# Performance work log

Measured on AMD Instinct MI355X. Metric: run time of the kernel, lower is better.

## Reference

```python
import jax, jax.numpy as jnp
import numpy as np

L = 4      # num_layers
H = 8      # nhead
D = 128    # d_model
FF = 256   # dim_feedforward
V = 16     # vocab_size
S = 1024   # window_size (== seq_len, mask is built at this size)
B = 8      # batch
LW = 128   # local attention window (+- LW)
EPS = 1e-5 # torch LayerNorm default


def setup_inputs() -> dict:
    key = jax.random.key(0)
    ks = jax.random.split(key, 8)
    n = lambda k, shape, s=0.02: jax.random.normal(k, shape, dtype=jnp.float32) * s
    return {
        "token_batch": jax.random.randint(ks[0], (B, S), 0, V, dtype=jnp.int32),
        "emb": n(ks[1], (V, D), 1.0),
        "Wqkv": n(ks[2], (L, 3 * D, D)), "bqkv": jnp.zeros((L, 3 * D)),
        "Wo": n(ks[3], (L, D, D)), "bo": jnp.zeros((L, D)),
        "ln1_g": jnp.ones((L, D)), "ln1_b": jnp.zeros((L, D)),
        "ln2_g": jnp.ones((L, D)), "ln2_b": jnp.zeros((L, D)),
        "W1": n(ks[4], (L, FF, D)), "b1": jnp.zeros((L, FF)),
        "W2": n(ks[5], (L, D, FF)), "b2": jnp.zeros((L, D)),
        "lnf_g": jnp.ones((D,)), "lnf_b": jnp.zeros((D,)),
        "Wout": n(ks[6], (1, D)), "bout": jnp.zeros((1,)),
    }


def _ln(x, g, b):
    m = jnp.mean(x, axis=-1, keepdims=True)
    v = jnp.var(x, axis=-1, keepdims=True)
    return (x - m) / jnp.sqrt(v + EPS) * g + b


def _pos_encoding(seq_len, d_model):
    pos = jnp.arange(seq_len, dtype=jnp.float32)[:, None]
    div = jnp.exp(jnp.arange(0, d_model, 2, dtype=jnp.float32) * (-jnp.log(10000.0) / d_model))
    pe = jnp.zeros((seq_len, d_model), dtype=jnp.float32)
    pe = pe.at[:, 0::2].set(jnp.sin(pos * div))
    pe = pe.at[:, 1::2].set(jnp.cos(pos * div))
    return pe


def reference(token_batch, emb, Wqkv, bqkv, Wo, bo, ln1_g, ln1_b, ln2_g, ln2_b,
              W1, b1, W2, b2, lnf_g, lnf_b, Wout, bout):
    Bn, Sn = token_batch.shape
    Dm = emb.shape[1]
    hd = Dm // H
    # embedding + sinusoidal positions (dropout is identity in eval mode)
    x = emb[token_batch] + _pos_encoding(Sn, Dm)[None]  # [B,S,D]
    # local band mask: 0 inside +-LW, -inf outside (as in _create_local_attention_mask)
    i = jnp.arange(Sn)
    mask = jnp.where(jnp.abs(i[:, None] - i[None, :]) <= LW, 0.0, -jnp.inf)  # [S,S]
    for l in range(Wqkv.shape[0]):
        # post-norm TransformerEncoderLayer, relu activation (torch defaults)
        qkv = x @ Wqkv[l].T + bqkv[l]
        q, k, v = jnp.split(qkv, 3, axis=-1)
        q = q.reshape(Bn, Sn, H, hd)
        k = k.reshape(Bn, Sn, H, hd)
        v = v.reshape(Bn, Sn, H, hd)
        scores = jnp.einsum('bqhd,bkhd->bhqk', q, k) / jnp.sqrt(jnp.float32(hd)) + mask
        attn = jax.nn.softmax(scores, axis=-1)
        ctx = jnp.einsum('bhqk,bkhd->bqhd', attn, v).reshape(Bn, Sn, Dm)
        x = _ln(x + ctx @ Wo[l].T + bo[l], ln1_g[l], ln1_b[l])
        ff = jax.nn.relu(x @ W1[l].T + b1[l]) @ W2[l].T + b2[l]
        x = _ln(x + ff, ln2_g[l], ln2_b[l])
    x = _ln(x, lnf_g, lnf_b)
    out = jax.nn.softplus(x @ Wout.T + bout)  # [B,S,1]
    return out[..., 0]
```

## Files before the change

### kernel.cpp

```cpp
#include <hip/hip_runtime.h>
#include <hip/hip_bf16.h>
#include <math.h>

#define NL   4
#define NH   8
#define DM   128
#define FFD  256
#define SEQ  1024
#define BATCH 8
#define NT   (BATCH*SEQ)
#define EPSV 1e-5f

typedef _Float16 h16;
typedef h16   h16x8 __attribute__((ext_vector_type(8)));
typedef float f32x4 __attribute__((ext_vector_type(4)));

#define WQKV_OFF 0
#define WO_OFF   196608
#define W1_OFF   262144
#define W2_OFF   393216
#define WTOT     524288

__global__ __launch_bounds__(256) void cvtw_kernel(
    const float* __restrict__ wqkv, const float* __restrict__ wo,
    const float* __restrict__ w1, const float* __restrict__ w2,
    h16* __restrict__ dst)
{
    int i = (blockIdx.x * 256 + threadIdx.x) * 4;
    const float* src; int off;
    if (i < WO_OFF)      { src = wqkv; off = 0; }
    else if (i < W1_OFF) { src = wo;   off = WO_OFF; }
    else if (i < W2_OFF) { src = w1;   off = W1_OFF; }
    else                 { src = w2;   off = W2_OFF; }
    float4 v = *(const float4*)&src[i - off];
    h16 o[4] = {(h16)v.x, (h16)v.y, (h16)v.z, (h16)v.w};
    *(uint2*)&dst[i] = *(uint2*)o;
}

__global__ __launch_bounds__(256) void embed_kernel(
    const int* __restrict__ tok, const float* __restrict__ emb,
    float* __restrict__ x, h16* __restrict__ xh)
{
    int idx = blockIdx.x * 256 + threadIdx.x;
    int t = idx >> 7;
    int d = idx & 127;
    int s = t & (SEQ - 1);
    int token = tok[t];
    float freq = expf((float)(d & ~1) * (-9.210340371976184f / 128.0f));
    float ang = (float)s * freq;
    float pe = (d & 1) ? cosf(ang) : sinf(ang);
    float v = emb[token * DM + d] + pe;
    x[idx] = v;
    xh[idx] = (h16)v;
}

__global__ __launch_bounds__(256) void gemm16_kernel(
    const h16* __restrict__ A, const h16* __restrict__ W,
    const float* __restrict__ bias, h16* __restrict__ out16, int N)
{
    __shared__ h16 Al[64 * 136];
    __shared__ h16 Wl[64 * 136];

    int tid = threadIdx.x;
    long row0 = (long)blockIdx.x * 64;
    long col0 = (long)blockIdx.y * 64;

    for (int idx = tid; idx < 64 * 16; idx += 256) {
        int r = idx >> 4, c = idx & 15;
        *(uint4*)&Al[r * 136 + c * 8] = *(const uint4*)&A[(row0 + r) * 128 + c * 8];
        *(uint4*)&Wl[r * 136 + c * 8] = *(const uint4*)&W[(col0 + r) * 128 + c * 8];
    }
    __syncthreads();

    int lane = tid & 63, wv = tid >> 6;
    int lr = lane & 15, lg = lane >> 4;
    int wr = (wv >> 1) * 32, wc = (wv & 1) * 32;

    f32x4 acc[2][2] = {{{0.f,0.f,0.f,0.f},{0.f,0.f,0.f,0.f}},
                       {{0.f,0.f,0.f,0.f},{0.f,0.f,0.f,0.f}}};

    #pragma unroll
    for (int k0 = 0; k0 < 128; k0 += 32) {
        h16x8 a0 = *(const h16x8*)&Al[(wr +      lr) * 136 + k0 + lg * 8];
        h16x8 a1 = *(const h16x8*)&Al[(wr + 16 + lr) * 136 + k0 + lg * 8];
        h16x8 b0 = *(const h16x8*)&Wl[(wc +      lr) * 136 + k0 + lg * 8];
        h16x8 b1 = *(const h16x8*)&Wl[(wc + 16 + lr) * 136 + k0 + lg * 8];
        acc[0][0] = __builtin_amdgcn_mfma_f32_16x16x32_f16(a0, b0, acc[0][0], 0, 0, 0);
        acc[0][1] = __builtin_amdgcn_mfma_f32_16x16x32_f16(a0, b1, acc[0][1], 0, 0, 0);
        acc[1][0] = __builtin_amdgcn_mfma_f32_16x16x32_f16(a1, b0, acc[1][0], 0, 0, 0);
        acc[1][1] = __builtin_amdgcn_mfma_f32_16x16x32_f16(a1, b1, acc[1][1], 0, 0, 0);
    }

    #pragma unroll
    for (int m = 0; m < 2; ++m)
    #pragma unroll
    for (int n = 0; n < 2; ++n) {
        long col = col0 + wc + 16 * n + lr;
        float bv = bias[col];
        #pragma unroll
        for (int r = 0; r < 4; ++r) {
            long row = row0 + wr + 16 * m + lg * 4 + r;
            out16[row * N + col] = (h16)(acc[m][n][r] + bv);
        }
    }
}

__device__ __forceinline__ void ln_epilogue(
    f32x4 acc[4], long row0, int wrow, int wcol, int lg, int lr, int w,
    const float* __restrict__ bias, const float* __restrict__ g,
    const float* __restrict__ bb, const float* __restrict__ xres,
    float* __restrict__ xo, h16* __restrict__ xho, float (*red)[2][2])
{
    float val[4][4];
    float bv[4];
    #pragma unroll
    for (int n = 0; n < 4; ++n) bv[n] = bias[wcol + 16 * n + lr];
    #pragma unroll
    for (int r = 0; r < 4; ++r) {
        long row = row0 + wrow + lg * 4 + r;
        #pragma unroll
        for (int n = 0; n < 4; ++n)
            val[r][n] = acc[n][r] + bv[n] + xres[row * 128 + wcol + 16 * n + lr];
    }
    float s[4], sq[4];
    #pragma unroll
    for (int r = 0; r < 4; ++r) {
        s[r]  = val[r][0] + val[r][1] + val[r][2] + val[r][3];
        sq[r] = val[r][0]*val[r][0] + val[r][1]*val[r][1]
              + val[r][2]*val[r][2] + val[r][3]*val[r][3];
        #pragma unroll
        for (int m = 1; m < 16; m <<= 1) {
            s[r]  += __shfl_xor(s[r], m);
            sq[r] += __shfl_xor(sq[r], m);
        }
    }
    int cg = w & 1;
    if (lr == 0) {
        #pragma unroll
        for (int r = 0; r < 4; ++r) {
            red[wrow + lg * 4 + r][cg][0] = s[r];
            red[wrow + lg * 4 + r][cg][1] = sq[r];
        }
    }
    __syncthreads();
    #pragma unroll
    for (int r = 0; r < 4; ++r) {
        int rowt = wrow + lg * 4 + r;
        float S  = red[rowt][0][0] + red[rowt][1][0];
        float SQ = red[rowt][0][1] + red[rowt][1][1];
        float mean = S * (1.0f / 128.0f);
        float var  = SQ * (1.0f / 128.0f) - mean * mean;
        float rstd = rsqrtf(var + EPSV);
        long row = row0 + rowt;
        #pragma unroll
        for (int n = 0; n < 4; ++n) {
            int col = wcol + 16 * n + lr;
            float o = (val[r][n] - mean) * rstd * g[col] + bb[col];
            xo[row * 128 + col]  = o;
            xho[row * 128 + col] = (h16)o;
        }
    }
}

__global__ __launch_bounds__(256) void wo_ln_kernel(
    const h16* __restrict__ ctx, const h16* __restrict__ Wo,
    const float* __restrict__ bo,
    const float* __restrict__ g, const float* __restrict__ bb,
    float* __restrict__ x, h16* __restrict__ xh)
{
    __shared__ h16 Xl[32 * 136];
    __shared__ h16 Wl[128 * 136];
    __shared__ float red[32][2][2];

    int tid = threadIdx.x;
    long row0 = (long)blockIdx.x * 32;

    for (int idx = tid; idx < 32 * 16; idx += 256) {
        int r = idx >> 4, c = idx & 15;
        *(uint4*)&Xl[r * 136 + c * 8] = *(const uint4*)&ctx[(row0 + r) * 128 + c * 8];
    }
    for (int idx = tid; idx < 128 * 16; idx += 256) {
        int r = idx >> 4, c = idx & 15;
        *(uint4*)&Wl[r * 136 + c * 8] = *(const uint4*)&Wo[r * 128 + c * 8];
    }
    __syncthreads();

    int lane = tid & 63, w = tid >> 6;
    int lr = lane & 15, lg = lane >> 4;
    int wrow = (w >> 1) * 16, wcol = (w & 1) * 64;

    f32x4 acc[4] = {{0.f,0.f,0.f,0.f},{0.f,0.f,0.f,0.f},
                    {0.f,0.f,0.f,0.f},{0.f,0.f,0.f,0.f}};
    #pragma unroll
    for (int k0 = 0; k0 < 128; k0 += 32) {
        h16x8 af = *(const h16x8*)&Xl[(wrow + lr) * 136 + k0 + lg * 8];
        #pragma unroll
        for (int n = 0; n < 4; ++n) {
            h16x8 bf = *(const h16x8*)&Wl[(wcol + 16 * n + lr) * 136 + k0 + lg * 8];
            acc[n] = __builtin_amdgcn_mfma_f32_16x16x32_f16(af, bf, acc[n], 0, 0, 0);
        }
    }

    ln_epilogue(acc, row0, wrow, wcol, lg, lr, w, bo, g, bb, x, x, xh, red);
}

__global__ __launch_bounds__(256) void ff_ln_kernel(
    const h16* __restrict__ xh_in, const float* __restrict__ xres,
    const h16* __restrict__ W1, const float* __restrict__ b1,
    const h16* __restrict__ W2, const float* __restrict__ b2,
    const float* __restrict__ g, const float* __restrict__ bb,
    float* __restrict__ x_out, h16* __restrict__ xh_out)
{
    __shared__ h16 Xl[32 * 136];
    __shared__ h16 Wl[128 * 136];
    __shared__ h16 Al[32 * 136];
    __shared__ float red[32][2][2];

    int tid = threadIdx.x;
    long row0 = (long)blockIdx.x * 32;

    for (int idx = tid; idx < 32 * 16; idx += 256) {
        int r = idx >> 4, c = idx & 15;
        *(uint4*)&Xl[r * 136 + c * 8] = *(const uint4*)&xh_in[(row0 + r) * 128 + c * 8];
    }

    int lane = tid & 63, w = tid >> 6;
    int lr = lane & 15, lg = lane >> 4;
    int wrow = (w >> 1) * 16, wcol = (w & 1) * 64;

    f32x4 acc2[4] = {{0.f,0.f,0.f,0.f},{0.f,0.f,0.f,0.f},
                     {0.f,0.f,0.f,0.f},{0.f,0.f,0.f,0.f}};

    #pragma unroll 1
    for (int half = 0; half < 2; ++half) {
        __syncthreads();
        for (int idx = tid; idx < 128 * 16; idx += 256) {
            int r = idx >> 4, c = idx & 15;
            *(uint4*)&Wl[r * 136 + c * 8] =
                *(const uint4*)&W1[(128 * half + r) * 128 + c * 8];
        }
        __syncthreads();

        f32x4 acc1[4] = {{0.f,0.f,0.f,0.f},{0.f,0.f,0.f,0.f},
                         {0.f,0.f,0.f,0.f},{0.f,0.f,0.f,0.f}};
        #pragma unroll
        for (int k0 = 0; k0 < 128; k0 += 32) {
            h16x8 af = *(const h16x8*)&Xl[(wrow + lr) * 136 + k0 + lg * 8];
            #pragma unroll
            for (int n = 0; n < 4; ++n) {
                h16x8 bf = *(const h16x8*)&Wl[(wcol + 16 * n + lr) * 136 + k0 + lg * 8];
                acc1[n] = __builtin_amdgcn_mfma_f32_16x16x32_f16(af, bf, acc1[n], 0, 0, 0);
            }
        }
        __syncthreads();

        #pragma unroll
        for (int r = 0; r < 4; ++r)
            #pragma unroll
            for (int n = 0; n < 4; ++n) {
                int col = wcol + 16 * n + lr;
                float v = acc1[n][r] + b1[128 * half + col];
                Al[(wrow + lg * 4 + r) * 136 + col] = (h16)fmaxf(v, 0.f);
            }
        for (int idx = tid; idx < 128 * 16; idx += 256) {
            int r = idx >> 4, c = idx & 15;
            *(uint4*)&Wl[r * 136 + c * 8] =
                *(const uint4*)&W2[r * 256 + 128 * half + c * 8];
        }
        __syncthreads();

        #pragma unroll
        for (int k0 = 0; k0 < 128; k0 += 32) {
            h16x8 af = *(const h16x8*)&Al[(wrow + lr) * 136 + k0 + lg * 8];
            #pragma unroll
            for (int n = 0; n < 4; ++n) {
                h16x8 bf = *(const h16x8*)&Wl[(wcol + 16 * n + lr) * 136 + k0 + lg * 8];
                acc2[n] = __builtin_amdgcn_mfma_f32_16x16x32_f16(af, bf, acc2[n], 0, 0, 0);
            }
        }
    }

    ln_epilogue(acc2, row0, wrow, wcol, lg, lr, w, b2, g, bb, xres, x_out, xh_out, red);
}

#define NSLOT 336
#define KSTR  24
#define VSTR  344
#define PSTR  296

__global__ __launch_bounds__(256) void attn16_kernel(
    const h16* __restrict__ qkvh, h16* __restrict__ ctxh)
{
    __shared__ h16 Kl[NSLOT * KSTR];
    __shared__ h16 Vt[16 * VSTR];
    __shared__ h16 Pl[4 * 16 * PSTR];

    int tid = threadIdx.x;
    int blk = blockIdx.x;
    int qb = blk & 15;
    int h  = (blk >> 4) & 7;
    int b  = blk >> 7;
    int q0b = qb * 64;
    int kw0 = q0b - 128;

    for (int idx = tid; idx < NSLOT * 2; idx += 256) {
        int slot = idx >> 1, part = (idx & 1) * 8;
        int ka = kw0 + slot;
        uint4 val = {0u, 0u, 0u, 0u};
        if (ka >= 0 && ka < SEQ)
            val = *(const uint4*)&qkvh[((size_t)(b * SEQ + ka)) * 384 + h * 16 + 128 + part];
        *(uint4*)&Kl[slot * KSTR + part] = val;
    }
    for (int idx = tid; idx < NSLOT * 2; idx += 256) {
        int slot = idx >> 1, part = (idx & 1) * 8;
        int ka = kw0 + slot;
        uint4 val = {0u, 0u, 0u, 0u};
        if (ka >= 0 && ka < SEQ)
            val = *(const uint4*)&qkvh[((size_t)(b * SEQ + ka)) * 384 + h * 16 + 256 + part];
        h16 tmp[8];
        *(uint4*)tmp = val;
        #pragma unroll
        for (int j = 0; j < 8; ++j)
            Vt[(part + j) * VSTR + slot] = tmp[j];
    }
    __syncthreads();

    int lane = tid & 63, w = tid >> 6;
    int lr = lane & 15, lg = lane >> 4;
    int q0w = q0b + w * 16;

    h16x8 qf = {0, 0, 0, 0, 0, 0, 0, 0};
    if (lg < 2)
        qf = *(const h16x8*)&qkvh[((size_t)(b * SEQ + q0w + lr)) * 384 + h * 16 + lg * 8];
    qf = qf * (h16)0.25f;

    f32x4 s[17];
    const f32x4 zero4 = {0.f, 0.f, 0.f, 0.f};
    #pragma unroll
    for (int t = 0; t < 17; ++t) {
        h16x8 kf = {0, 0, 0, 0, 0, 0, 0, 0};
        if (lg < 2)
            kf = *(const h16x8*)&Kl[(w * 16 + t * 16 + lr) * KSTR + lg * 8];
        s[t] = __builtin_amdgcn_mfma_f32_16x16x32_f16(qf, kf, zero4, 0, 0, 0);
    }

    bool interior = (q0b >= 128) && (q0b <= 832);
    if (interior) {
        #pragma unroll
        for (int r = 0; r < 4; ++r) {
            int qr = lg * 4 + r;
            if (lr < qr) s[0][r]  = -1e30f;
            if (lr > qr) s[16][r] = -1e30f;
        }
    } else {
        #pragma unroll
        for (int t = 0; t < 17; ++t)
        #pragma unroll
        for (int r = 0; r < 4; ++r) {
            int rel = 16 * t + lr - (lg * 4 + r);
            int ka  = kw0 + w * 16 + 16 * t + lr;
            bool valid = (rel >= 0) && (rel <= 256) && (ka >= 0) && (ka < SEQ);
            if (!valid) s[t][r] = -1e30f;
        }
    }

    float mx[4] = {-1e30f, -1e30f, -1e30f, -1e30f};
    #pragma unroll
    for (int t = 0; t < 17; ++t)
        #pragma unroll
        for (int r = 0; r < 4; ++r) mx[r] = fmaxf(mx[r], s[t][r]);
    #pragma unroll
    for (int r = 0; r < 4; ++r) {
        mx[r] = fmaxf(mx[r], __shfl_xor(mx[r], 1));
        mx[r] = fmaxf(mx[r], __shfl_xor(mx[r], 2));
        mx[r] = fmaxf(mx[r], __shfl_xor(mx[r], 4));
        mx[r] = fmaxf(mx[r], __shfl_xor(mx[r], 8));
    }
    float sum[4] = {0.f, 0.f, 0.f, 0.f};
    #pragma unroll
    for (int t = 0; t < 17; ++t)
        #pragma unroll
        for (int r = 0; r < 4; ++r) {
            float p = __expf(s[t][r] - mx[r]);
            s[t][r] = p;
            sum[r] += p;
        }
    #pragma unroll
    for (int r = 0; r < 4; ++r) {
        sum[r] += __shfl_xor(sum[r], 1);
        sum[r] += __shfl_xor(sum[r], 2);
        sum[r] += __shfl_xor(sum[r], 4);
        sum[r] += __shfl_xor(sum[r], 8);
    }

    h16* Pw = &Pl[w * 16 * PSTR];
    #pragma unroll
    for (int t = 0; t < 17; ++t)
        #pragma unroll
        for (int r = 0; r < 4; ++r)
            Pw[(lg * 4 + r) * PSTR + t * 16 + lr] = (h16)s[t][r];
    #pragma unroll
    for (int r = 0; r < 4; ++r)
        Pw[(lg * 4 + r) * PSTR + 272 + lr] = (h16)0.f;

    f32x4 o = {0.f, 0.f, 0.f, 0.f};
    #pragma unroll
    for (int c = 0; c < 9; ++c) {
        h16x8 pf = *(const h16x8*)&Pw[lr * PSTR + c * 32 + lg * 8];
        h16x8 vf = *(const h16x8*)&Vt[lr * VSTR + w * 16 + c * 32 + lg * 8];
        o = __builtin_amdgcn_mfma_f32_16x16x32_f16(pf, vf, o, 0, 0, 0);
    }

    #pragma unroll
    for (int r = 0; r < 4; ++r) {
        float val = o[r] / sum[r];
        ctxh[((size_t)(b * SEQ + q0w + lg * 4 + r)) * DM + h * 16 + lr] = (h16)val;
    }
}

__global__ __launch_bounds__(256) void final_kernel(
    const float* __restrict__ x, const float* __restrict__ g,
    const float* __restrict__ bb, const float* __restrict__ Wout,
    const float* __restrict__ bout, float* __restrict__ out)
{
    int wave = threadIdx.x >> 6;
    int lane = threadIdx.x & 63;
    int row = blockIdx.x * 4 + wave;
    size_t base = (size_t)row * DM + lane * 2;

    float2 xv = *(const float2*)&x[base];
    float a = xv.x, c = xv.y;
    float s = a + c, sq = a * a + c * c;
    #pragma unroll
    for (int m = 1; m < 64; m <<= 1) {
        s  += __shfl_xor(s, m);
        sq += __shfl_xor(sq, m);
    }
    float mean = s * (1.0f / 128.0f);
    float var = sq * (1.0f / 128.0f) - mean * mean;
    float rstd = rsqrtf(var + EPSV);
    float2 gv = *(const float2*)&g[lane * 2];
    float2 bv = *(const float2*)&bb[lane * 2];
    float na = (a - mean) * rstd * gv.x + bv.x;
    float nc = (c - mean) * rstd * gv.y + bv.y;

    float2 wv = *(const float2*)&Wout[lane * 2];
    float d = na * wv.x + nc * wv.y;
    #pragma unroll
    for (int m = 1; m < 64; m <<= 1) d += __shfl_xor(d, m);

    if (lane == 0) {
        float z = d + bout[0];
        out[row] = fmaxf(z, 0.f) + log1pf(__expf(-fabsf(z)));
    }
}

extern "C" void kernel_launch(void* const* d_in, const int* in_sizes, int n_in,
                              void* d_out, int out_size, void* d_ws, size_t ws_size,
                              hipStream_t stream)
{
    const int*   tok  = (const int*)d_in[0];
    const float* emb  = (const float*)d_in[1];
    const float* Wqkv = (const float*)d_in[2];
    const float* bqkv = (const float*)d_in[3];
    const float* Wo   = (const float*)d_in[4];
    const float* bo   = (const float*)d_in[5];
    const float* ln1g = (const float*)d_in[6];
    const float* ln1b = (const float*)d_in[7];
    const float* ln2g = (const float*)d_in[8];
    const float* ln2b = (const float*)d_in[9];
    const float* W1   = (const float*)d_in[10];
    const float* b1   = (const float*)d_in[11];
    const float* W2   = (const float*)d_in[12];
    const float* b2   = (const float*)d_in[13];
    const float* lnfg = (const float*)d_in[14];
    const float* lnfb = (const float*)d_in[15];
    const float* Wout = (const float*)d_in[16];
    const float* bout = (const float*)d_in[17];
    float* out = (float*)d_out;

    char* wsb = (char*)d_ws;
    float* x    = (float*)wsb;
    h16*   xh   = (h16*)(wsb + 4194304);
    h16*   qkvh = (h16*)(wsb + 6291456);
    h16*   ctxh = (h16*)(wsb + 12582912);
    h16*   wh   = (h16*)(wsb + 14680064);

    h16* Wqkv_h = wh + WQKV_OFF;
    h16* Wo_h   = wh + WO_OFF;
    h16* W1_h   = wh + W1_OFF;
    h16* W2_h   = wh + W2_OFF;

    cvtw_kernel<<<WTOT / 4 / 256, 256, 0, stream>>>(Wqkv, Wo, W1, W2, wh);
    embed_kernel<<<NT * DM / 256, 256, 0, stream>>>(tok, emb, x, xh);

    for (int l = 0; l < NL; ++l) {
        gemm16_kernel<<<dim3(NT / 64, 384 / 64), 256, 0, stream>>>(
            xh, Wqkv_h + (size_t)l * 384 * 128, bqkv + l * 384, qkvh, 384);
        attn16_kernel<<<BATCH * NH * (SEQ / 64), 256, 0, stream>>>(qkvh, ctxh);
        wo_ln_kernel<<<NT / 32, 256, 0, stream>>>(
            ctxh, Wo_h + (size_t)l * 128 * 128, bo + l * 128,
            ln1g + l * DM, ln1b + l * DM, x, xh);
        ff_ln_kernel<<<NT / 32, 256, 0, stream>>>(
            xh, x,
            W1_h + (size_t)l * 256 * 128, b1 + l * 256,
            W2_h + (size_t)l * 128 * 256, b2 + l * 128,
            ln2g + l * DM, ln2b + l * DM, x, xh);
    }

    final_kernel<<<NT / 4, 256, 0, stream>>>(x, lnfg, lnfb, Wout, bout, out);
}
```

Measured before the change: 259.0 us.

## Fuse Wo+LN1, FFN+LN2 and final head into one tail kernel; merge prep kernels

Merges the out-projection+LN1 and FFN+LN2 kernels into one tail kernel per layer. The LN1 output stays in registers and LDS instead of being written to global memory and reread. On the last layer the final LayerNorm, output projection and softplus are folded in, and the weight conversion and embedding kernels are combined into one launch. This removes launches and global round-trips of x/xh, but the tail kernel carries more registers and barriers.

```diff
diff --git a/kernel.cpp b/kernel.cpp
--- a/kernel.cpp
+++ b/kernel.cpp
@@ -21,37 +21,37 @@
 #define W2_OFF   393216
 #define WTOT     524288
 
-__global__ __launch_bounds__(256) void cvtw_kernel(
+__global__ __launch_bounds__(256) void prep_kernel(
+    const int* __restrict__ tok, const float* __restrict__ emb,
+    float* __restrict__ x, h16* __restrict__ xh,
     const float* __restrict__ wqkv, const float* __restrict__ wo,
     const float* __restrict__ w1, const float* __restrict__ w2,
-    h16* __restrict__ dst)
+    h16* __restrict__ wdst)
 {
-    int i = (blockIdx.x * 256 + threadIdx.x) * 4;
-    const float* src; int off;
-    if (i < WO_OFF)      { src = wqkv; off = 0; }
-    else if (i < W1_OFF) { src = wo;   off = WO_OFF; }
-    else if (i < W2_OFF) { src = w1;   off = W1_OFF; }
-    else                 { src = w2;   off = W2_OFF; }
-    float4 v = *(const float4*)&src[i - off];
-    h16 o[4] = {(h16)v.x, (h16)v.y, (h16)v.z, (h16)v.w};
-    *(uint2*)&dst[i] = *(uint2*)o;
-}
-
-__global__ __launch_bounds__(256) void embed_kernel(
-    const int* __restrict__ tok, const float* __restrict__ emb,
-    float* __restrict__ x, h16* __restrict__ xh)
-{
-    int idx = blockIdx.x * 256 + threadIdx.x;
-    int t = idx >> 7;
-    int d = idx & 127;
-    int s = t & (SEQ - 1);
-    int token = tok[t];
-    float freq = expf((float)(d & ~1) * (-9.210340371976184f / 128.0f));
-    float ang = (float)s * freq;
-    float pe = (d & 1) ? cosf(ang) : sinf(ang);
-    float v = emb[token * DM + d] + pe;
-    x[idx] = v;
-    xh[idx] = (h16)v;
+    int bid = blockIdx.x;
+    if (bid < 4096) {
+        int idx = bid * 256 + threadIdx.x;
+        int t = idx >> 7;
+        int d = idx & 127;
+        int s = t & (SEQ - 1);
+        int token = tok[t];
+        float freq = expf((float)(d & ~1) * (-9.210340371976184f / 128.0f));
+        float ang = (float)s * freq;
+        float pe = (d & 1) ? cosf(ang) : sinf(ang);
+        float v = emb[token * DM + d] + pe;
+        x[idx] = v;
+        xh[idx] = (h16)v;
+    } else {
+        int i = ((bid - 4096) * 256 + threadIdx.x) * 4;
+        const float* src; int off;
+        if (i < WO_OFF)      { src = wqkv; off = 0; }
+        else if (i < W1_OFF) { src = wo;   off = WO_OFF; }
+        else if (i < W2_OFF) { src = w1;   off = W1_OFF; }
+        else                 { src = w2;   off = W2_OFF; }
+        float4 v = *(const float4*)&src[i - off];
+        h16 o[4] = {(h16)v.x, (h16)v.y, (h16)v.z, (h16)v.w};
+        *(uint2*)&wdst[i] = *(uint2*)o;
+    }
 }
 
 __global__ __launch_bounds__(256) void gemm16_kernel(
@@ -105,184 +105,6 @@
     }
 }
 
-__device__ __forceinline__ void ln_epilogue(
-    f32x4 acc[4], long row0, int wrow, int wcol, int lg, int lr, int w,
-    const float* __restrict__ bias, const float* __restrict__ g,
-    const float* __restrict__ bb, const float* __restrict__ xres,
-    float* __restrict__ xo, h16* __restrict__ xho, float (*red)[2][2])
-{
-    float val[4][4];
-    float bv[4];
-    #pragma unroll
-    for (int n = 0; n < 4; ++n) bv[n] = bias[wcol + 16 * n + lr];
-    #pragma unroll
-    for (int r = 0; r < 4; ++r) {
-        long row = row0 + wrow + lg * 4 + r;
-        #pragma unroll
-        for (int n = 0; n < 4; ++n)
-            val[r][n] = acc[n][r] + bv[n] + xres[row * 128 + wcol + 16 * n + lr];
-    }
-    float s[4], sq[4];
-    #pragma unroll
-    for (int r = 0; r < 4; ++r) {
-        s[r]  = val[r][0] + val[r][1] + val[r][2] + val[r][3];
-        sq[r] = val[r][0]*val[r][0] + val[r][1]*val[r][1]
-              + val[r][2]*val[r][2] + val[r][3]*val[r][3];
-        #pragma unroll
-        for (int m = 1; m < 16; m <<= 1) {
-            s[r]  += __shfl_xor(s[r], m);
-            sq[r] += __shfl_xor(sq[r], m);
-        }
-    }
-    int cg = w & 1;
-    if (lr == 0) {
-        #pragma unroll
-        for (int r = 0; r < 4; ++r) {
-            red[wrow + lg * 4 + r][cg][0] = s[r];
-            red[wrow + lg * 4 + r][cg][1] = sq[r];
-        }
-    }
-    __syncthreads();
-    #pragma unroll
-    for (int r = 0; r < 4; ++r) {
-        int rowt = wrow + lg * 4 + r;
-        float S  = red[rowt][0][0] + red[rowt][1][0];
-        float SQ = red[rowt][0][1] + red[rowt][1][1];
-        float mean = S * (1.0f / 128.0f);
-        float var  = SQ * (1.0f / 128.0f) - mean * mean;
-        float rstd = rsqrtf(var + EPSV);
-        long row = row0 + rowt;
-        #pragma unroll
-        for (int n = 0; n < 4; ++n) {
-            int col = wcol + 16 * n + lr;
-            float o = (val[r][n] - mean) * rstd * g[col] + bb[col];
-            xo[row * 128 + col]  = o;
-            xho[row * 128 + col] = (h16)o;
-        }
-    }
-}
-
-__global__ __launch_bounds__(256) void wo_ln_kernel(
-    const h16* __restrict__ ctx, const h16* __restrict__ Wo,
-    const float* __restrict__ bo,
-    const float* __restrict__ g, const float* __restrict__ bb,
-    float* __restrict__ x, h16* __restrict__ xh)
-{
-    __shared__ h16 Xl[32 * 136];
-    __shared__ h16 Wl[128 * 136];
-    __shared__ float red[32][2][2];
-
-    int tid = threadIdx.x;
-    long row0 = (long)blockIdx.x * 32;
-
-    for (int idx = tid; idx < 32 * 16; idx += 256) {
-        int r = idx >> 4, c = idx & 15;
-        *(uint4*)&Xl[r * 136 + c * 8] = *(const uint4*)&ctx[(row0 + r) * 128 + c * 8];
-    }
-    for (int idx = tid; idx < 128 * 16; idx += 256) {
-        int r = idx >> 4, c = idx & 15;
-        *(uint4*)&Wl[r * 136 + c * 8] = *(const uint4*)&Wo[r * 128 + c * 8];
-    }
-    __syncthreads();
-
-    int lane = tid & 63, w = tid >> 6;
-    int lr = lane & 15, lg = lane >> 4;
-    int wrow = (w >> 1) * 16, wcol = (w & 1) * 64;
-
-    f32x4 acc[4] = {{0.f,0.f,0.f,0.f},{0.f,0.f,0.f,0.f},
-                    {0.f,0.f,0.f,0.f},{0.f,0.f,0.f,0.f}};
-    #pragma unroll
-    for (int k0 = 0; k0 < 128; k0 += 32) {
-        h16x8 af = *(const h16x8*)&Xl[(wrow + lr) * 136 + k0 + lg * 8];
-        #pragma unroll
-        for (int n = 0; n < 4; ++n) {
-            h16x8 bf = *(const h16x8*)&Wl[(wcol + 16 * n + lr) * 136 + k0 + lg * 8];
-            acc[n] = __builtin_amdgcn_mfma_f32_16x16x32_f16(af, bf, acc[n], 0, 0, 0);
-        }
-    }
-
-    ln_epilogue(acc, row0, wrow, wcol, lg, lr, w, bo, g, bb, x, x, xh, red);
-}
-
-__global__ __launch_bounds__(256) void ff_ln_kernel(
-    const h16* __restrict__ xh_in, const float* __restrict__ xres,
-    const h16* __restrict__ W1, const float* __restrict__ b1,
-    const h16* __restrict__ W2, const float* __restrict__ b2,
-    const float* __restrict__ g, const float* __restrict__ bb,
-    float* __restrict__ x_out, h16* __restrict__ xh_out)
-{
-    __shared__ h16 Xl[32 * 136];
-    __shared__ h16 Wl[128 * 136];
-    __shared__ h16 Al[32 * 136];
-    __shared__ float red[32][2][2];
-
-    int tid = threadIdx.x;
-    long row0 = (long)blockIdx.x * 32;
-
-    for (int idx = tid; idx < 32 * 16; idx += 256) {
-        int r = idx >> 4, c = idx & 15;
-        *(uint4*)&Xl[r * 136 + c * 8] = *(const uint4*)&xh_in[(row0 + r) * 128 + c * 8];
-    }
-
-    int lane = tid & 63, w = tid >> 6;
-    int lr = lane & 15, lg = lane >> 4;
-    int wrow = (w >> 1) * 16, wcol = (w & 1) * 64;
-
-    f32x4 acc2[4] = {{0.f,0.f,0.f,0.f},{0.f,0.f,0.f,0.f},
-                     {0.f,0.f,0.f,0.f},{0.f,0.f,0.f,0.f}};
-
-    #pragma unroll 1
-    for (int half = 0; half < 2; ++half) {
-        __syncthreads();
-        for (int idx = tid; idx < 128 * 16; idx += 256) {
-            int r = idx >> 4, c = idx & 15;
-            *(uint4*)&Wl[r * 136 + c * 8] =
-                *(const uint4*)&W1[(128 * half + r) * 128 + c * 8];
-        }
-        __syncthreads();
-
-        f32x4 acc1[4] = {{0.f,0.f,0.f,0.f},{0.f,0.f,0.f,0.f},
-                         {0.f,0.f,0.f,0.f},{0.f,0.f,0.f,0.f}};
-        #pragma unroll
-        for (int k0 = 0; k0 < 128; k0 += 32) {
-            h16x8 af = *(const h16x8*)&Xl[(wrow + lr) * 136 + k0 + lg * 8];
-            #pragma unroll
-            for (int n = 0; n < 4; ++n) {
-                h16x8 bf = *(const h16x8*)&Wl[(wcol + 16 * n + lr) * 136 + k0 + lg * 8];
-                acc1[n] = __builtin_amdgcn_mfma_f32_16x16x32_f16(af, bf, acc1[n], 0, 0, 0);
-            }
-        }
-        __syncthreads();
-
-        #pragma unroll
-        for (int r = 0; r < 4; ++r)
-            #pragma unroll
-            for (int n = 0; n < 4; ++n) {
-                int col = wcol + 16 * n + lr;
-                float v = acc1[n][r] + b1[128 * half + col];
-                Al[(wrow + lg * 4 + r) * 136 + col] = (h16)fmaxf(v, 0.f);
-            }
-        for (int idx = tid; idx < 128 * 16; idx += 256) {
-            int r = idx >> 4, c = idx & 15;
-            *(uint4*)&Wl[r * 136 + c * 8] =
-                *(const uint4*)&W2[r * 256 + 128 * half + c * 8];
-        }
-        __syncthreads();
-
-        #pragma unroll
-        for (int k0 = 0; k0 < 128; k0 += 32) {
-            h16x8 af = *(const h16x8*)&Al[(wrow + lr) * 136 + k0 + lg * 8];
-            #pragma unroll
-            for (int n = 0; n < 4; ++n) {
-                h16x8 bf = *(const h16x8*)&Wl[(wcol + 16 * n + lr) * 136 + k0 + lg * 8];
-                acc2[n] = __builtin_amdgcn_mfma_f32_16x16x32_f16(af, bf, acc2[n], 0, 0, 0);
-            }
-        }
-    }
-
-    ln_epilogue(acc2, row0, wrow, wcol, lg, lr, w, b2, g, bb, xres, x_out, xh_out, red);
-}
-
 #define NSLOT 336
 #define KSTR  24
 #define VSTR  344
@@ -418,40 +240,249 @@
     }
 }
 
-__global__ __launch_bounds__(256) void final_kernel(
-    const float* __restrict__ x, const float* __restrict__ g,
-    const float* __restrict__ bb, const float* __restrict__ Wout,
-    const float* __restrict__ bout, float* __restrict__ out)
+template<int LAST>
+__global__ __launch_bounds__(256) void tail_kernel(
+    const h16* __restrict__ ctx, const float* __restrict__ xres,
+    const h16* __restrict__ Wo, const float* __restrict__ bo,
+    const float* __restrict__ g1, const float* __restrict__ bb1,
+    const h16* __restrict__ W1, const float* __restrict__ b1,
+    const h16* __restrict__ W2, const float* __restrict__ b2,
+    const float* __restrict__ g2, const float* __restrict__ bb2,
+    const float* __restrict__ gf, const float* __restrict__ bf,
+    const float* __restrict__ Wout, const float* __restrict__ bout,
+    float* __restrict__ x_out, h16* __restrict__ xh_out,
+    float* __restrict__ out)
 {
-    int wave = threadIdx.x >> 6;
-    int lane = threadIdx.x & 63;
-    int row = blockIdx.x * 4 + wave;
-    size_t base = (size_t)row * DM + lane * 2;
-
-    float2 xv = *(const float2*)&x[base];
-    float a = xv.x, c = xv.y;
-    float s = a + c, sq = a * a + c * c;
-    #pragma unroll
-    for (int m = 1; m < 64; m <<= 1) {
-        s  += __shfl_xor(s, m);
-        sq += __shfl_xor(sq, m);
-    }
-    float mean = s * (1.0f / 128.0f);
-    float var = sq * (1.0f / 128.0f) - mean * mean;
-    float rstd = rsqrtf(var + EPSV);
-    float2 gv = *(const float2*)&g[lane * 2];
-    float2 bv = *(const float2*)&bb[lane * 2];
-    float na = (a - mean) * rstd * gv.x + bv.x;
-    float nc = (c - mean) * rstd * gv.y + bv.y;
-
-    float2 wv = *(const float2*)&Wout[lane * 2];
-    float d = na * wv.x + nc * wv.y;
-    #pragma unroll
-    for (int m = 1; m < 64; m <<= 1) d += __shfl_xor(d, m);
-
-    if (lane == 0) {
-        float z = d + bout[0];
-        out[row] = fmaxf(z, 0.f) + log1pf(__expf(-fabsf(z)));
+    __shared__ h16 Xl[32 * 136];
+    __shared__ h16 Wl[128 * 136];
+    __shared__ h16 Al[32 * 136];
+    __shared__ float red[32][2][2];
+
+    int tid = threadIdx.x;
+    long row0 = (long)blockIdx.x * 32;
+
+    for (int idx = tid; idx < 32 * 16; idx += 256) {
+        int r = idx >> 4, c = idx & 15;
+        *(uint4*)&Xl[r * 136 + c * 8] = *(const uint4*)&ctx[(row0 + r) * 128 + c * 8];
+    }
+    for (int idx = tid; idx < 128 * 16; idx += 256) {
+        int r = idx >> 4, c = idx & 15;
+        *(uint4*)&Wl[r * 136 + c * 8] = *(const uint4*)&Wo[r * 128 + c * 8];
+    }
+    __syncthreads();
+
+    int lane = tid & 63, w = tid >> 6;
+    int lr = lane & 15, lg = lane >> 4;
+    int wrow = (w >> 1) * 16, wcol = (w & 1) * 64;
+    int cg = w & 1;
+
+    f32x4 acc[4] = {{0.f,0.f,0.f,0.f},{0.f,0.f,0.f,0.f},
+                    {0.f,0.f,0.f,0.f},{0.f,0.f,0.f,0.f}};
+    #pragma unroll
+    for (int k0 = 0; k0 < 128; k0 += 32) {
+        h16x8 af = *(const h16x8*)&Xl[(wrow + lr) * 136 + k0 + lg * 8];
+        #pragma unroll
+        for (int n = 0; n < 4; ++n) {
+            h16x8 bfr = *(const h16x8*)&Wl[(wcol + 16 * n + lr) * 136 + k0 + lg * 8];
+            acc[n] = __builtin_amdgcn_mfma_f32_16x16x32_f16(af, bfr, acc[n], 0, 0, 0);
+        }
+    }
+
+    float val1[4][4];
+    #pragma unroll
+    for (int r = 0; r < 4; ++r) {
+        long row = row0 + wrow + lg * 4 + r;
+        #pragma unroll
+        for (int n = 0; n < 4; ++n) {
+            int col = wcol + 16 * n + lr;
+            val1[r][n] = acc[n][r] + bo[col] + xres[row * 128 + col];
+        }
+    }
+    #pragma unroll
+    for (int r = 0; r < 4; ++r) {
+        float s  = val1[r][0] + val1[r][1] + val1[r][2] + val1[r][3];
+        float sq = val1[r][0]*val1[r][0] + val1[r][1]*val1[r][1]
+                 + val1[r][2]*val1[r][2] + val1[r][3]*val1[r][3];
+        #pragma unroll
+        for (int m = 1; m < 16; m <<= 1) {
+            s  += __shfl_xor(s, m);
+            sq += __shfl_xor(sq, m);
+        }
+        if (lr == 0) {
+            red[wrow + lg * 4 + r][cg][0] = s;
+            red[wrow + lg * 4 + r][cg][1] = sq;
+        }
+    }
+    __syncthreads();
+    #pragma unroll
+    for (int r = 0; r < 4; ++r) {
+        int rowt = wrow + lg * 4 + r;
+        float S  = red[rowt][0][0] + red[rowt][1][0];
+        float SQ = red[rowt][0][1] + red[rowt][1][1];
+        float mean = S * (1.0f / 128.0f);
+        float var  = SQ * (1.0f / 128.0f) - mean * mean;
+        float rstd = rsqrtf(var + EPSV);
+        #pragma unroll
+        for (int n = 0; n < 4; ++n) {
+            int col = wcol + 16 * n + lr;
+            val1[r][n] = (val1[r][n] - mean) * rstd * g1[col] + bb1[col];
+        }
+    }
+    #pragma unroll
+    for (int r = 0; r < 4; ++r)
+        #pragma unroll
+        for (int n = 0; n < 4; ++n)
+            Xl[(wrow + lg * 4 + r) * 136 + wcol + 16 * n + lr] = (h16)val1[r][n];
+
+    f32x4 acc2[4] = {{0.f,0.f,0.f,0.f},{0.f,0.f,0.f,0.f},
+                     {0.f,0.f,0.f,0.f},{0.f,0.f,0.f,0.f}};
+
+    #pragma unroll 1
+    for (int half = 0; half < 2; ++half) {
+        for (int idx = tid; idx < 128 * 16; idx += 256) {
+            int r = idx >> 4, c = idx & 15;
+            *(uint4*)&Wl[r * 136 + c * 8] =
+                *(const uint4*)&W1[(long)(128 * half + r) * 128 + c * 8];
+        }
+        __syncthreads();
+
+        f32x4 a1[4] = {{0.f,0.f,0.f,0.f},{0.f,0.f,0.f,0.f},
+                       {0.f,0.f,0.f,0.f},{0.f,0.f,0.f,0.f}};
+        #pragma unroll
+        for (int k0 = 0; k0 < 128; k0 += 32) {
+            h16x8 af = *(const h16x8*)&Xl[(wrow + lr) * 136 + k0 + lg * 8];
+            #pragma unroll
+            for (int n = 0; n < 4; ++n) {
+                h16x8 bfr = *(const h16x8*)&Wl[(wcol + 16 * n + lr) * 136 + k0 + lg * 8];
+                a1[n] = __builtin_amdgcn_mfma_f32_16x16x32_f16(af, bfr, a1[n], 0, 0, 0);
+            }
+        }
+        __syncthreads();
+
+        #pragma unroll
+        for (int r = 0; r < 4; ++r)
+            #pragma unroll
+            for (int n = 0; n < 4; ++n) {
+                int col = wcol + 16 * n + lr;
+                float v = a1[n][r] + b1[128 * half + col];
+                Al[(wrow + lg * 4 + r) * 136 + col] = (h16)fmaxf(v, 0.f);
+            }
+        for (int idx = tid; idx < 128 * 16; idx += 256) {
+            int r = idx >> 4, c = idx & 15;
+            *(uint4*)&Wl[r * 136 + c * 8] =
+                *(const uint4*)&W2[(long)r * 256 + 128 * half + c * 8];
+        }
+        __syncthreads();
+
+        #pragma unroll
+        for (int k0 = 0; k0 < 128; k0 += 32) {
+            h16x8 af = *(const h16x8*)&Al[(wrow + lr) * 136 + k0 + lg * 8];
+            #pragma unroll
+            for (int n = 0; n < 4; ++n) {
+                h16x8 bfr = *(const h16x8*)&Wl[(wcol + 16 * n + lr) * 136 + k0 + lg * 8];
+                acc2[n] = __builtin_amdgcn_mfma_f32_16x16x32_f16(af, bfr, acc2[n], 0, 0, 0);
+            }
+        }
+        __syncthreads();
+    }
+
+    float val2[4][4];
+    #pragma unroll
+    for (int r = 0; r < 4; ++r)
+        #pragma unroll
+        for (int n = 0; n < 4; ++n) {
+            int col = wcol + 16 * n + lr;
+            val2[r][n] = acc2[n][r] + b2[col] + val1[r][n];
+        }
+    #pragma unroll
+    for (int r = 0; r < 4; ++r) {
+        float s  = val2[r][0] + val2[r][1] + val2[r][2] + val2[r][3];
+        float sq = val2[r][0]*val2[r][0] + val2[r][1]*val2[r][1]
+                 + val2[r][2]*val2[r][2] + val2[r][3]*val2[r][3];
+        #pragma unroll
+        for (int m = 1; m < 16; m <<= 1) {
+            s  += __shfl_xor(s, m);
+            sq += __shfl_xor(sq, m);
+        }
+        if (lr == 0) {
+            red[wrow + lg * 4 + r][cg][0] = s;
+            red[wrow + lg * 4 + r][cg][1] = sq;
+        }
+    }
+    __syncthreads();
+    #pragma unroll
+    for (int r = 0; r < 4; ++r) {
+        int rowt = wrow + lg * 4 + r;
+        float S  = red[rowt][0][0] + red[rowt][1][0];
+        float SQ = red[rowt][0][1] + red[rowt][1][1];
+        float mean = S * (1.0f / 128.0f);
+        float var  = SQ * (1.0f / 128.0f) - mean * mean;
+        float rstd = rsqrtf(var + EPSV);
+        #pragma unroll
+        for (int n = 0; n < 4; ++n) {
+            int col = wcol + 16 * n + lr;
+            val2[r][n] = (val2[r][n] - mean) * rstd * g2[col] + bb2[col];
+        }
+    }
+
+    if (!LAST) {
+        #pragma unroll
+        for (int r = 0; r < 4; ++r) {
+            long row = row0 + wrow + lg * 4 + r;
+            #pragma unroll
+            for (int n = 0; n < 4; ++n) {
+                int col = wcol + 16 * n + lr;
+                x_out[row * 128 + col]  = val2[r][n];
+                xh_out[row * 128 + col] = (h16)val2[r][n];
+            }
+        }
+    } else {
+        __syncthreads();
+        #pragma unroll
+        for (int r = 0; r < 4; ++r) {
+            float s  = val2[r][0] + val2[r][1] + val2[r][2] + val2[r][3];
+            float sq = val2[r][0]*val2[r][0] + val2[r][1]*val2[r][1]
+                     + val2[r][2]*val2[r][2] + val2[r][3]*val2[r][3];
+            #pragma unroll
+            for (int m = 1; m < 16; m <<= 1) {
+                s  += __shfl_xor(s, m);
+                sq += __shfl_xor(sq, m);
+            }
+            if (lr == 0) {
+                red[wrow + lg * 4 + r][cg][0] = s;
+                red[wrow + lg * 4 + r][cg][1] = sq;
+            }
+        }
+        __syncthreads();
+        float dotp[4];
+        #pragma unroll
+        for (int r = 0; r < 4; ++r) {
+            int rowt = wrow + lg * 4 + r;
+            float S  = red[rowt][0][0] + red[rowt][1][0];
+            float SQ = red[rowt][0][1] + red[rowt][1][1];
+            float mean = S * (1.0f / 128.0f);
+            float var  = SQ * (1.0f / 128.0f) - mean * mean;
+            float rstd = rsqrtf(var + EPSV);
+            float d = 0.f;
+            #pragma unroll
+            for (int n = 0; n < 4; ++n) {
+                int col = wcol + 16 * n + lr;
+                float nf = (val2[r][n] - mean) * rstd * gf[col] + bf[col];
+                d = fmaf(nf, Wout[col], d);
+            }
+            #pragma unroll
+            for (int m = 1; m < 16; m <<= 1) d += __shfl_xor(d, m);
+            dotp[r] = d;
+        }
+        __syncthreads();
+        #pragma unroll
+        for (int r = 0; r < 4; ++r)
+            if (lr == 0) red[wrow + lg * 4 + r][cg][0] = dotp[r];
+        __syncthreads();
+        if (tid < 32) {
+            float z = red[tid][0][0] + red[tid][1][0] + bout[0];
+            out[row0 + tid] = fmaxf(z, 0.f) + log1pf(__expf(-fabsf(z)));
+        }
     }
 }
 
@@ -491,22 +522,33 @@
     h16* W1_h   = wh + W1_OFF;
     h16* W2_h   = wh + W2_OFF;
 
-    cvtw_kernel<<<WTOT / 4 / 256, 256, 0, stream>>>(Wqkv, Wo, W1, W2, wh);
-    embed_kernel<<<NT * DM / 256, 256, 0, stream>>>(tok, emb, x, xh);
+    prep_kernel<<<4096 + WTOT / 1024, 256, 0, stream>>>(
+        tok, emb, x, xh, Wqkv, Wo, W1, W2, wh);
 
     for (int l = 0; l < NL; ++l) {
         gemm16_kernel<<<dim3(NT / 64, 384 / 64), 256, 0, stream>>>(
             xh, Wqkv_h + (size_t)l * 384 * 128, bqkv + l * 384, qkvh, 384);
         attn16_kernel<<<BATCH * NH * (SEQ / 64), 256, 0, stream>>>(qkvh, ctxh);
-        wo_ln_kernel<<<NT / 32, 256, 0, stream>>>(
-            ctxh, Wo_h + (size_t)l * 128 * 128, bo + l * 128,
-            ln1g + l * DM, ln1b + l * DM, x, xh);
-        ff_ln_kernel<<<NT / 32, 256, 0, stream>>>(
-            xh, x,
-            W1_h + (size_t)l * 256 * 128, b1 + l * 256,
-            W2_h + (size_t)l * 128 * 256, b2 + l * 128,
-            ln2g + l * DM, ln2b + l * DM, x, xh);
-    }
-
-    final_kernel<<<NT / 4, 256, 0, stream>>>(x, lnfg, lnfb, Wout, bout, out);
+        if (l < NL - 1) {
+            tail_kernel<0><<<NT / 32, 256, 0, stream>>>(
+                ctxh, x,
+                Wo_h + (size_t)l * 128 * 128, bo + l * 128,
+                ln1g + l * DM, ln1b + l * DM,
+                W1_h + (size_t)l * 256 * 128, b1 + l * 256,
+                W2_h + (size_t)l * 128 * 256, b2 + l * 128,
+                ln2g + l * DM, ln2b + l * DM,
+                lnfg, lnfb, Wout, bout,
+                x, xh, out);
+        } else {
+            tail_kernel<1><<<NT / 32, 256, 0, stream>>>(
+                ctxh, x,
+                Wo_h + (size_t)l * 128 * 128, bo + l * 128,
+                ln1g + l * DM, ln1b + l * DM,
+                W1_h + (size_t)l * 256 * 128, b1 + l * 256,
+                W2_h + (size_t)l * 128 * 256, b2 + l * 128,
+                ln2g + l * DM, ln2b + l * DM,
+                lnfg, lnfb, Wout, bout,
+                x, xh, out);
+        }
+    }
 }
```

New measurement: 245.1 us. 5.4% less time.
